# Performance work log

Measured on AMD Instinct MI355X. Metric: run time of the kernel, lower is better.

The kernel has to match this reference:

```python
import jax, jax.numpy as jnp
import numpy as np

N, F_IN, H, D = 4096, 256, 4, 64  # out_features = H*D = 256
SLOPE = 0.2
LN_EPS = 1e-5


def setup_inputs() -> dict:
    key = jax.random.key(0)
    k1, k2, k3, k4 = jax.random.split(key, 4)
    x = jax.random.normal(k1, (N, F_IN), dtype=jnp.float32)
    adjacency = jax.random.bernoulli(k2, 0.5, (N, N))
    # xavier_uniform for W [H*D, F_IN] and a [H, 2*D]
    lim_w = float(np.sqrt(6.0 / (F_IN + H * D)))
    W = jax.random.uniform(k3, (H * D, F_IN), minval=-lim_w, maxval=lim_w, dtype=jnp.float32)
    lim_a = float(np.sqrt(6.0 / (H + 2 * D)))
    a = jax.random.uniform(k4, (H, 2 * D), minval=-lim_a, maxval=lim_a, dtype=jnp.float32)
    ln_gamma = jnp.ones((H * D,), dtype=jnp.float32)
    ln_beta = jnp.zeros((H * D,), dtype=jnp.float32)
    return {"x": x, "adjacency": adjacency, "W": W, "a": a,
            "ln_gamma": ln_gamma, "ln_beta": ln_beta}


def _layernorm(y, gamma, beta):
    mu = jnp.mean(y, axis=-1, keepdims=True)
    var = jnp.mean((y - mu) ** 2, axis=-1, keepdims=True)
    return (y - mu) * jax.lax.rsqrt(var + LN_EPS) * gamma + beta


def reference(x, adjacency, W, a, ln_gamma, ln_beta):
    # Wx: [N, H, D]
    Wx = (x @ W.T).reshape(N, H, D)
    # Additive score split: sum over concat([Wx_i, Wx_j]) * a == Wx_i.a_src + Wx_j.a_dst
    a_src, a_dst = a[:, :D], a[:, D:]
    s_i = jnp.einsum('nhd,hd->nh', Wx, a_src)  # [N, H] (destination i)
    s_j = jnp.einsum('nhd,hd->nh', Wx, a_dst)  # [N, H] (source j)
    e = s_i[:, None, :] + s_j[None, :, :]       # [N, N, H]
    e = jnp.where(e >= 0, e, SLOPE * e)          # leaky relu
    e = jnp.where(adjacency[:, :, None], e, -jnp.inf)
    attn = jax.nn.softmax(e, axis=1)             # softmax over source j (dim=1)
    # dropout is identity in eval mode
    out = jnp.einsum('ijh,jhd->ihd', attn, Wx).reshape(N, H * D)
    out = out + x  # out_features == in_features -> residual
    return _layernorm(out, ln_gamma, ln_beta)
```

## Files before the change

### kernel.cpp

```cpp
#include <hip/hip_runtime.h>
#include <hip/hip_bf16.h>
#include <cstdint>
#include <cstddef>

#define N_NODES 4096
#define F_IN    256
#define H_HEADS 4
#define D_HEAD  64
#define FEAT    256
#define SLOPE   0.2f
#define LN_EPS  1e-5f

#define NCHUNK  4
#define J_CHUNK 1024
#define I_TILE  32
#define K_STEP  32
#define NSTEP   (J_CHUNK / K_STEP)

typedef __attribute__((ext_vector_type(8))) short bf16x8;
typedef __attribute__((ext_vector_type(4))) float f32x4;

#define FLAG_OFF   0
#define GMAX_OFF   64
#define ADJB_OFF   256
#define ADJB_BYTES ((size_t)N_NODES * 128 * 4)
#define WXT_OFF    (ADJB_OFF + ADJB_BYTES)
#define WXT_BYTES  ((size_t)FEAT * N_NODES * 2)
#define SSRC_OFF   (WXT_OFF + WXT_BYTES)
#define SVEC_BYTES ((size_t)H_HEADS * N_NODES * 4)
#define SDST_OFF   (SSRC_OFF + SVEC_BYTES)
#define WSL_OFF    (SDST_OFF + SVEC_BYTES)
#define WSL_BYTES  ((size_t)NCHUNK * N_NODES * H_HEADS * 4)
#define WSACC_OFF  (WSL_OFF + WSL_BYTES)
#define WSACC_BYTES ((size_t)NCHUNK * N_NODES * FEAT * 4)

__device__ __forceinline__ short f2bf(float f) {
    uint32_t u = __float_as_uint(f);
    uint32_t r = (u + 0x7fffu + ((u >> 16) & 1u)) >> 16;
    return (short)r;
}
__device__ __forceinline__ uint32_t fkey(float f) {
    uint32_t u = __float_as_uint(f);
    return ((int)u < 0) ? ~u : (u | 0x80000000u);
}
__device__ __forceinline__ float funkey(uint32_t k) {
    uint32_t u = (k & 0x80000000u) ? (k & 0x7fffffffu) : ~k;
    return __uint_as_float(u);
}

__global__ void detect_kernel(const uint8_t* __restrict__ adj,
                              int* __restrict__ flag, uint32_t* __restrict__ gmax) {
    int t = threadIdx.x;
    uint32_t acc = 0;
    for (int idx = t; idx < 4096; idx += 64)
        if (idx & 3) acc |= adj[idx];
    unsigned long long any = __ballot(acc != 0);
    if (t == 0) *flag = (any == 0ull) ? 1 : 0;
    if (t < H_HEADS) gmax[t] = 0u;
}

__global__ __launch_bounds__(256) void pack_adj(const uint8_t* __restrict__ adj8,
                                                const int* __restrict__ flag,
                                                uint32_t* __restrict__ bits) {
    int gid = blockIdx.x * 256 + threadIdx.x;
    uint32_t b = 0;
    if (!(*flag)) {
        const uint32_t* src = (const uint32_t*)adj8 + (size_t)gid * 8;
        #pragma unroll
        for (int k = 0; k < 8; ++k) {
            uint32_t v = src[k];
            if (v & 0x000000ffu) b |= 1u << (k * 4 + 0);
            if (v & 0x0000ff00u) b |= 1u << (k * 4 + 1);
            if (v & 0x00ff0000u) b |= 1u << (k * 4 + 2);
            if (v & 0xff000000u) b |= 1u << (k * 4 + 3);
        }
    } else {
        const int4* src = (const int4*)adj8 + (size_t)gid * 8;
        #pragma unroll
        for (int k = 0; k < 8; ++k) {
            int4 v = src[k];
            if (v.x) b |= 1u << (k * 4 + 0);
            if (v.y) b |= 1u << (k * 4 + 1);
            if (v.z) b |= 1u << (k * 4 + 2);
            if (v.w) b |= 1u << (k * 4 + 3);
        }
    }
    bits[gid] = b;
}

__global__ __launch_bounds__(256) void gemm_wx(const float* __restrict__ x,
                                               const float* __restrict__ W,
                                               const float* __restrict__ a,
                                               short* __restrict__ WxT,
                                               float* __restrict__ s_srcT,
                                               float* __restrict__ s_dstT,
                                               uint32_t* __restrict__ gmax) {
    __shared__ float xs[64][68];
    __shared__ float wsm[64][68];
    __shared__ float aS[64], aD[64];
    __shared__ float wredmax[4];
    const int h  = blockIdx.x;
    const int nt = blockIdx.y;
    const int t  = threadIdx.x;
    const int tm = t >> 4, tn = t & 15;
    if (t < 64)       aS[t]      = a[h * 128 + t];
    else if (t < 128) aD[t - 64] = a[h * 128 + 64 + (t - 64)];
    float acc[4][4] = {};

    for (int k0 = 0; k0 < F_IN; k0 += 64) {
        #pragma unroll
        for (int s = 0; s < 4; ++s) {
            int idx = t + s * 256;
            int r = idx >> 4, c4 = (idx & 15) << 2;
            *(float4*)&xs[r][c4]  = *(const float4*)&x[(size_t)(nt * 64 + r) * F_IN + k0 + c4];
            *(float4*)&wsm[r][c4] = *(const float4*)&W[(size_t)(h * 64 + r) * F_IN + k0 + c4];
        }
        __syncthreads();
        #pragma unroll 4
        for (int kk = 0; kk < 64; ++kk) {
            float av[4], bv[4];
            #pragma unroll
            for (int mi = 0; mi < 4; ++mi) av[mi] = xs[tm * 4 + mi][kk];
            #pragma unroll
            for (int ni = 0; ni < 4; ++ni) bv[ni] = wsm[tn * 4 + ni][kk];
            #pragma unroll
            for (int mi = 0; mi < 4; ++mi)
                #pragma unroll
                for (int ni = 0; ni < 4; ++ni)
                    acc[mi][ni] = fmaf(av[mi], bv[ni], acc[mi][ni]);
        }
        __syncthreads();
    }

    #pragma unroll
    for (int ni = 0; ni < 4; ++ni) {
        short4 sv;
        sv.x = f2bf(acc[0][ni]); sv.y = f2bf(acc[1][ni]);
        sv.z = f2bf(acc[2][ni]); sv.w = f2bf(acc[3][ni]);
        *(short4*)&WxT[(size_t)(h * 64 + tn * 4 + ni) * N_NODES + nt * 64 + tm * 4] = sv;
    }

    float ps[4] = {0.f, 0.f, 0.f, 0.f}, pd[4] = {0.f, 0.f, 0.f, 0.f};
    #pragma unroll
    for (int mi = 0; mi < 4; ++mi)
        #pragma unroll
        for (int ni = 0; ni < 4; ++ni) {
            float v = acc[mi][ni];
            ps[mi] = fmaf(v, aS[tn * 4 + ni], ps[mi]);
            pd[mi] = fmaf(v, aD[tn * 4 + ni], pd[mi]);
        }
    #pragma unroll
    for (int o = 1; o < 16; o <<= 1) {
        #pragma unroll
        for (int mi = 0; mi < 4; ++mi) {
            ps[mi] += __shfl_xor(ps[mi], o, 64);
            pd[mi] += __shfl_xor(pd[mi], o, 64);
        }
    }
    float lmax = -INFINITY;
    if (tn == 0) {
        #pragma unroll
        for (int mi = 0; mi < 4; ++mi) {
            int node = nt * 64 + tm * 4 + mi;
            s_srcT[(size_t)h * N_NODES + node] = ps[mi];
            s_dstT[(size_t)h * N_NODES + node] = pd[mi];
            lmax = fmaxf(lmax, pd[mi]);
        }
    }
    #pragma unroll
    for (int o = 1; o < 64; o <<= 1) lmax = fmaxf(lmax, __shfl_xor(lmax, o, 64));
    if ((t & 63) == 0) wredmax[t >> 6] = lmax;
    __syncthreads();
    if (t == 0) {
        float m = fmaxf(fmaxf(wredmax[0], wredmax[1]), fmaxf(wredmax[2], wredmax[3]));
        atomicMax(&gmax[h], fkey(m));
    }
}

__global__ __launch_bounds__(512, 4) void attn_chunk(const short* __restrict__ WxT,
                                                     const float* __restrict__ s_srcT,
                                                     const float* __restrict__ s_dstT,
                                                     const uint32_t* __restrict__ adjbits,
                                                     const uint32_t* __restrict__ gmax,
                                                     float* __restrict__ ws_l,
                                                     float* __restrict__ ws_acc) {
    __shared__ short    Bt[2][256][40];
    __shared__ uint32_t adjW[32][33];
    __shared__ float    sJ[4][1032];

    const int t     = threadIdx.x;
    const int tile  = blockIdx.x >> 2;
    const int chunk = blockIdx.x & 3;
    const int i0    = tile * I_TILE;
    const int jc    = chunk * J_CHUNK;
    const int wave  = t >> 6, lane = t & 63;
    const int h     = wave & 3, mh = wave >> 2;
    const int col   = lane & 15, q = lane >> 4;

    for (int s2 = t; s2 < 1024; s2 += 512)
        adjW[s2 >> 5][s2 & 31] =
            adjbits[(size_t)(i0 + (s2 >> 5)) * 128 + chunk * 32 + (s2 & 31)];
    for (int s2 = t; s2 < 1024; s2 += 512) {
        int pl = s2 >> 8, off = (s2 & 255) * 4;
        *(float4*)&sJ[pl][off] = *(const float4*)&s_dstT[(size_t)pl * N_NODES + jc + off];
    }
    const int sf = t >> 1, shalf = t & 1;
    const int4* gsrc = (const int4*)(WxT + (size_t)sf * N_NODES + jc);
    {
        int4 v0 = gsrc[shalf * 2 + 0], v1 = gsrc[shalf * 2 + 1];
        int4* ld = (int4*)&Bt[0][sf][shalf * 16];
        ld[0] = v0; ld[1] = v1;
    }
    __syncthreads();

    const int   iL  = mh * 16 + col;
    const int   i   = i0 + iL;
    const float si  = s_srcT[(size_t)h * N_NODES + i];
    const float gm  = funkey(gmax[h]);
    const float em0 = si + gm;
    const float mi_ = fmaxf(em0, SLOPE * em0);

    f32x4 cacc[4], cl;
    #pragma unroll
    for (int n = 0; n < 4; ++n)
        #pragma unroll
        for (int r2 = 0; r2 < 4; ++r2) cacc[n][r2] = 0.f;
    #pragma unroll
    for (int r2 = 0; r2 < 4; ++r2) cl[r2] = 0.f;

    bf16x8 onesf;
    #pragma unroll
    for (int e = 0; e < 8; ++e) onesf[e] = (col == 0) ? (short)0x3F80 : (short)0;

    for (int ks = 0; ks < NSTEP; ++ks) {
        const int  cur  = ks & 1;
        const bool more = (ks + 1 < NSTEP);
        int4 pf0, pf1;
        if (more) {
            pf0 = gsrc[(ks + 1) * 4 + shalf * 2 + 0];
            pf1 = gsrc[(ks + 1) * 4 + shalf * 2 + 1];
        }

        uint32_t wq = adjW[iL][ks] >> (q * 8);
        const float4 sa = *(const float4*)&sJ[h][ks * 32 + q * 8];
        const float4 sb = *(const float4*)&sJ[h][ks * 32 + q * 8 + 4];
        float sjv[8] = {sa.x, sa.y, sa.z, sa.w, sb.x, sb.y, sb.z, sb.w};
        bf16x8 ap;
        #pragma unroll
        for (int jj = 0; jj < 8; ++jj) {
            float e = si + sjv[jj];
            e = fmaxf(e, SLOPE * e);
            float p = __expf(e - mi_);
            p = (wq & (1u << jj)) ? p : 0.f;
            ap[jj] = f2bf(p);
        }

        #pragma unroll
        for (int n = 0; n < 4; ++n) {
            bf16x8 bfr = *(const bf16x8*)&Bt[cur][h * 64 + n * 16 + col][q * 8];
            cacc[n] = __builtin_amdgcn_mfma_f32_16x16x32_bf16(ap, bfr, cacc[n], 0, 0, 0);
        }
        cl = __builtin_amdgcn_mfma_f32_16x16x32_bf16(ap, onesf, cl, 0, 0, 0);

        if (more) {
            int4* ld = (int4*)&Bt[cur ^ 1][sf][shalf * 16];
            ld[0] = pf0; ld[1] = pf1;
        }
        __syncthreads();
    }

    #pragma unroll
    for (int n = 0; n < 4; ++n)
        #pragma unroll
        for (int r = 0; r < 4; ++r) {
            int ii = i0 + mh * 16 + q * 4 + r;
            ws_acc[((size_t)chunk * N_NODES + ii) * FEAT + h * 64 + n * 16 + col] = cacc[n][r];
        }
    if (col == 0) {
        #pragma unroll
        for (int r = 0; r < 4; ++r) {
            int ii = i0 + mh * 16 + q * 4 + r;
            ws_l[((size_t)chunk * N_NODES + ii) * H_HEADS + h] = cl[r];
        }
    }
}

__global__ __launch_bounds__(256) void finalize_kernel(const float* __restrict__ x,
                                                       const float* __restrict__ gamma,
                                                       const float* __restrict__ beta,
                                                       const float* __restrict__ ws_l,
                                                       const float* __restrict__ ws_acc,
                                                       float* __restrict__ out) {
    const int i = blockIdx.x;
    const int t = threadIdx.x;
    const int h = t >> 6;
    const int lane = t & 63;

    float L = 0.f, y = 0.f;
    #pragma unroll
    for (int c = 0; c < NCHUNK; ++c) {
        L += ws_l[((size_t)c * N_NODES + i) * H_HEADS + h];
        y += ws_acc[((size_t)c * N_NODES + i) * FEAT + t];
    }
    y = (L > 0.f ? y / L : 0.f) + x[(size_t)i * FEAT + t];

    float s1 = y, s2 = y * y;
    #pragma unroll
    for (int o = 32; o > 0; o >>= 1) {
        s1 += __shfl_xor(s1, o, 64);
        s2 += __shfl_xor(s2, o, 64);
    }
    __shared__ float red1[4], red2[4];
    if (lane == 0) { red1[h] = s1; red2[h] = s2; }
    __syncthreads();
    s1 = red1[0] + red1[1] + red1[2] + red1[3];
    s2 = red2[0] + red2[1] + red2[2] + red2[3];
    float mu  = s1 * (1.f / 256.f);
    float var = s2 * (1.f / 256.f) - mu * mu;
    float r = 1.0f / sqrtf(var + LN_EPS);
    out[(size_t)i * FEAT + t] = (y - mu) * r * gamma[t] + beta[t];
}

extern "C" void kernel_launch(void* const* d_in, const int* in_sizes, int n_in,
                              void* d_out, int out_size, void* d_ws, size_t ws_size,
                              hipStream_t stream) {
    const float* x     = (const float*)d_in[0];
    const void*  adj   = d_in[1];
    const float* W     = (const float*)d_in[2];
    const float* a     = (const float*)d_in[3];
    const float* gamma = (const float*)d_in[4];
    const float* beta  = (const float*)d_in[5];
    float* out = (float*)d_out;

    char* ws = (char*)d_ws;
    int*      flag    = (int*)(ws + FLAG_OFF);
    uint32_t* gmax    = (uint32_t*)(ws + GMAX_OFF);
    uint32_t* adjbits = (uint32_t*)(ws + ADJB_OFF);
    short*    WxT     = (short*)(ws + WXT_OFF);
    float*    s_srcT  = (float*)(ws + SSRC_OFF);
    float*    s_dstT  = (float*)(ws + SDST_OFF);
    float*    ws_l    = (float*)(ws + WSL_OFF);
    float*    ws_acc  = (float*)(ws + WSACC_OFF);

    detect_kernel<<<1, 64, 0, stream>>>((const uint8_t*)adj, flag, gmax);
    pack_adj<<<2048, 256, 0, stream>>>((const uint8_t*)adj, flag, adjbits);
    gemm_wx<<<dim3(4, 64), 256, 0, stream>>>(x, W, a, WxT, s_srcT, s_dstT, gmax);
    attn_chunk<<<512, 512, 0, stream>>>(WxT, s_srcT, s_dstT, adjbits, gmax, ws_l, ws_acc);
    finalize_kernel<<<N_NODES, 256, 0, stream>>>(x, gamma, beta, ws_l, ws_acc, out);
}
```

Baseline: 183.7 us.

## Factor attention exponentials, drop detect kernel, deepen prefetch, vectorize GEMM and finalize

The attention kernel no longer computes exp per edge. Each weight is rebuilt as a product of per-node factors precomputed in the GEMM: exp(s_dst) and exp(0.2*s_dst) per source, plus Ai, A2i and a sign threshold per destination. The adjacency-format detection moves into pack_adj with a block-local check, removing one launch. WxT prefetch becomes two steps ahead, the GEMM inner loop reads float4 from shared memory, and finalize handles one row per wavefront with float4 accesses. The risks are exp overflow or underflow in the factored form, and a block-local dtype check that could misclassify a block whose adjacency is stored as bytes.

```diff
diff --git a/kernel.cpp b/kernel.cpp
--- a/kernel.cpp
+++ b/kernel.cpp
@@ -20,7 +20,6 @@
 typedef __attribute__((ext_vector_type(8))) short bf16x8;
 typedef __attribute__((ext_vector_type(4))) float f32x4;
 
-#define FLAG_OFF   0
 #define GMAX_OFF   64
 #define ADJB_OFF   256
 #define ADJB_BYTES ((size_t)N_NODES * 128 * 4)
@@ -28,11 +27,11 @@
 #define WXT_BYTES  ((size_t)FEAT * N_NODES * 2)
 #define SSRC_OFF   (WXT_OFF + WXT_BYTES)
 #define SVEC_BYTES ((size_t)H_HEADS * N_NODES * 4)
-#define SDST_OFF   (SSRC_OFF + SVEC_BYTES)
-#define WSL_OFF    (SDST_OFF + SVEC_BYTES)
+#define ETAB_OFF   (SSRC_OFF + SVEC_BYTES)
+#define ETAB_BYTES ((size_t)H_HEADS * N_NODES * 8)
+#define WSL_OFF    (ETAB_OFF + ETAB_BYTES)
 #define WSL_BYTES  ((size_t)NCHUNK * N_NODES * H_HEADS * 4)
 #define WSACC_OFF  (WSL_OFF + WSL_BYTES)
-#define WSACC_BYTES ((size_t)NCHUNK * N_NODES * FEAT * 4)
 
 __device__ __forceinline__ short f2bf(float f) {
     uint32_t u = __float_as_uint(f);
@@ -48,34 +47,39 @@
     return __uint_as_float(u);
 }
 
-__global__ void detect_kernel(const uint8_t* __restrict__ adj,
-                              int* __restrict__ flag, uint32_t* __restrict__ gmax) {
-    int t = threadIdx.x;
-    uint32_t acc = 0;
-    for (int idx = t; idx < 4096; idx += 64)
-        if (idx & 3) acc |= adj[idx];
-    unsigned long long any = __ballot(acc != 0);
-    if (t == 0) *flag = (any == 0ull) ? 1 : 0;
-    if (t < H_HEADS) gmax[t] = 0u;
-}
-
-__global__ __launch_bounds__(256) void pack_adj(const uint8_t* __restrict__ adj8,
-                                                const int* __restrict__ flag,
-                                                uint32_t* __restrict__ bits) {
-    int gid = blockIdx.x * 256 + threadIdx.x;
+__global__ __launch_bounds__(256) void pack_adj(const void* __restrict__ adjv,
+                                                uint32_t* __restrict__ bits,
+                                                uint32_t* __restrict__ gmax) {
+    __shared__ int s_u8;
+    const int t   = threadIdx.x;
+    const int gid = blockIdx.x * 256 + t;
+    if (blockIdx.x == 0 && t < H_HEADS) gmax[t] = 0u;
+
+    uint32_t w8[8];
+    const uint32_t* src8 = (const uint32_t*)adjv + (size_t)gid * 8;
+    #pragma unroll
+    for (int k = 0; k < 8; ++k) w8[k] = src8[k];
+
+    uint32_t off = 0;
+    #pragma unroll
+    for (int k = 0; k < 8; ++k) off |= (w8[k] & 0xFFFFFF00u);
+    if (t == 0) s_u8 = 0;
+    __syncthreads();
+    if (off) s_u8 = 1;
+    __syncthreads();
+
     uint32_t b = 0;
-    if (!(*flag)) {
-        const uint32_t* src = (const uint32_t*)adj8 + (size_t)gid * 8;
+    if (s_u8) {
         #pragma unroll
         for (int k = 0; k < 8; ++k) {
-            uint32_t v = src[k];
+            uint32_t v = w8[k];
             if (v & 0x000000ffu) b |= 1u << (k * 4 + 0);
             if (v & 0x0000ff00u) b |= 1u << (k * 4 + 1);
             if (v & 0x00ff0000u) b |= 1u << (k * 4 + 2);
             if (v & 0xff000000u) b |= 1u << (k * 4 + 3);
         }
     } else {
-        const int4* src = (const int4*)adj8 + (size_t)gid * 8;
+        const int4* src = (const int4*)adjv + (size_t)gid * 8;
         #pragma unroll
         for (int k = 0; k < 8; ++k) {
             int4 v = src[k];
@@ -93,7 +97,7 @@
                                                const float* __restrict__ a,
                                                short* __restrict__ WxT,
                                                float* __restrict__ s_srcT,
-                                               float* __restrict__ s_dstT,
+                                               float2* __restrict__ etab,
                                                uint32_t* __restrict__ gmax) {
     __shared__ float xs[64][68];
     __shared__ float wsm[64][68];
@@ -117,17 +121,21 @@
         }
         __syncthreads();
         #pragma unroll 4
-        for (int kk = 0; kk < 64; ++kk) {
-            float av[4], bv[4];
+        for (int kq = 0; kq < 16; ++kq) {
+            float4 xa[4], wb[4];
             #pragma unroll
-            for (int mi = 0; mi < 4; ++mi) av[mi] = xs[tm * 4 + mi][kk];
+            for (int mi = 0; mi < 4; ++mi) xa[mi] = *(const float4*)&xs[tm * 4 + mi][kq * 4];
             #pragma unroll
-            for (int ni = 0; ni < 4; ++ni) bv[ni] = wsm[tn * 4 + ni][kk];
+            for (int ni = 0; ni < 4; ++ni) wb[ni] = *(const float4*)&wsm[tn + 16 * ni][kq * 4];
             #pragma unroll
             for (int mi = 0; mi < 4; ++mi)
                 #pragma unroll
-                for (int ni = 0; ni < 4; ++ni)
-                    acc[mi][ni] = fmaf(av[mi], bv[ni], acc[mi][ni]);
+                for (int ni = 0; ni < 4; ++ni) {
+                    acc[mi][ni] = fmaf(xa[mi].x, wb[ni].x, acc[mi][ni]);
+                    acc[mi][ni] = fmaf(xa[mi].y, wb[ni].y, acc[mi][ni]);
+                    acc[mi][ni] = fmaf(xa[mi].z, wb[ni].z, acc[mi][ni]);
+                    acc[mi][ni] = fmaf(xa[mi].w, wb[ni].w, acc[mi][ni]);
+                }
         }
         __syncthreads();
     }
@@ -137,7 +145,7 @@
         short4 sv;
         sv.x = f2bf(acc[0][ni]); sv.y = f2bf(acc[1][ni]);
         sv.z = f2bf(acc[2][ni]); sv.w = f2bf(acc[3][ni]);
-        *(short4*)&WxT[(size_t)(h * 64 + tn * 4 + ni) * N_NODES + nt * 64 + tm * 4] = sv;
+        *(short4*)&WxT[(size_t)(h * 64 + tn + 16 * ni) * N_NODES + nt * 64 + tm * 4] = sv;
     }
 
     float ps[4] = {0.f, 0.f, 0.f, 0.f}, pd[4] = {0.f, 0.f, 0.f, 0.f};
@@ -146,8 +154,8 @@
         #pragma unroll
         for (int ni = 0; ni < 4; ++ni) {
             float v = acc[mi][ni];
-            ps[mi] = fmaf(v, aS[tn * 4 + ni], ps[mi]);
-            pd[mi] = fmaf(v, aD[tn * 4 + ni], pd[mi]);
+            ps[mi] = fmaf(v, aS[tn + 16 * ni], ps[mi]);
+            pd[mi] = fmaf(v, aD[tn + 16 * ni], pd[mi]);
         }
     #pragma unroll
     for (int o = 1; o < 16; o <<= 1) {
@@ -163,7 +171,7 @@
         for (int mi = 0; mi < 4; ++mi) {
             int node = nt * 64 + tm * 4 + mi;
             s_srcT[(size_t)h * N_NODES + node] = ps[mi];
-            s_dstT[(size_t)h * N_NODES + node] = pd[mi];
+            etab[(size_t)h * N_NODES + node] = make_float2(__expf(pd[mi]), __expf(0.2f * pd[mi]));
             lmax = fmaxf(lmax, pd[mi]);
         }
     }
@@ -179,14 +187,14 @@
 
 __global__ __launch_bounds__(512, 4) void attn_chunk(const short* __restrict__ WxT,
                                                      const float* __restrict__ s_srcT,
-                                                     const float* __restrict__ s_dstT,
+                                                     const float2* __restrict__ etab,
                                                      const uint32_t* __restrict__ adjbits,
                                                      const uint32_t* __restrict__ gmax,
                                                      float* __restrict__ ws_l,
                                                      float* __restrict__ ws_acc) {
     __shared__ short    Bt[2][256][40];
     __shared__ uint32_t adjW[32][33];
-    __shared__ float    sJ[4][1032];
+    __shared__ float    EJ[4 * 2048];
 
     const int t     = threadIdx.x;
     const int tile  = blockIdx.x >> 2;
@@ -200,16 +208,22 @@
     for (int s2 = t; s2 < 1024; s2 += 512)
         adjW[s2 >> 5][s2 & 31] =
             adjbits[(size_t)(i0 + (s2 >> 5)) * 128 + chunk * 32 + (s2 & 31)];
-    for (int s2 = t; s2 < 1024; s2 += 512) {
-        int pl = s2 >> 8, off = (s2 & 255) * 4;
-        *(float4*)&sJ[pl][off] = *(const float4*)&s_dstT[(size_t)pl * N_NODES + jc + off];
-    }
+    {
+        const float4* esrc = (const float4*)etab;
+        for (int s2 = t; s2 < 2048; s2 += 512) {
+            int pl = s2 >> 9, off = s2 & 511;
+            *(float4*)&EJ[pl * 2048 + off * 4] = esrc[(size_t)pl * 2048 + (jc >> 1) + off];
+        }
+    }
+
     const int sf = t >> 1, shalf = t & 1;
     const int4* gsrc = (const int4*)(WxT + (size_t)sf * N_NODES + jc);
+    int4 pfA0, pfA1, pfB0, pfB1;
+    pfA0 = gsrc[shalf * 2 + 0];           pfA1 = gsrc[shalf * 2 + 1];
+    pfB0 = gsrc[4 + shalf * 2 + 0];       pfB1 = gsrc[4 + shalf * 2 + 1];
     {
-        int4 v0 = gsrc[shalf * 2 + 0], v1 = gsrc[shalf * 2 + 1];
         int4* ld = (int4*)&Bt[0][sf][shalf * 16];
-        ld[0] = v0; ld[1] = v1;
+        ld[0] = pfA0; ld[1] = pfA1;
     }
     __syncthreads();
 
@@ -219,6 +233,9 @@
     const float gm  = funkey(gmax[h]);
     const float em0 = si + gm;
     const float mi_ = fmaxf(em0, SLOPE * em0);
+    const float Ai  = __expf(si - mi_);
+    const float A2i = __expf(0.2f * si - mi_);
+    const float Ti  = __expf(-si);
 
     f32x4 cacc[4], cl;
     #pragma unroll
@@ -232,40 +249,51 @@
     #pragma unroll
     for (int e = 0; e < 8; ++e) onesf[e] = (col == 0) ? (short)0x3F80 : (short)0;
 
+    #pragma unroll 2
     for (int ks = 0; ks < NSTEP; ++ks) {
-        const int  cur  = ks & 1;
-        const bool more = (ks + 1 < NSTEP);
-        int4 pf0, pf1;
-        if (more) {
-            pf0 = gsrc[(ks + 1) * 4 + shalf * 2 + 0];
-            pf1 = gsrc[(ks + 1) * 4 + shalf * 2 + 1];
+        const int cur = ks & 1;
+
+        if (ks + 1 < NSTEP) {
+            int4* ld = (int4*)&Bt[cur ^ 1][sf][shalf * 16];
+            if (cur) { ld[0] = pfA0; ld[1] = pfA1; }
+            else     { ld[0] = pfB0; ld[1] = pfB1; }
+        }
+        if (ks + 2 < NSTEP) {
+            if (cur) { pfB0 = gsrc[(ks + 2) * 4 + shalf * 2]; pfB1 = gsrc[(ks + 2) * 4 + shalf * 2 + 1]; }
+            else     { pfA0 = gsrc[(ks + 2) * 4 + shalf * 2]; pfA1 = gsrc[(ks + 2) * 4 + shalf * 2 + 1]; }
         }
 
         uint32_t wq = adjW[iL][ks] >> (q * 8);
-        const float4 sa = *(const float4*)&sJ[h][ks * 32 + q * 8];
-        const float4 sb = *(const float4*)&sJ[h][ks * 32 + q * 8 + 4];
-        float sjv[8] = {sa.x, sa.y, sa.z, sa.w, sb.x, sb.y, sb.z, sb.w};
-        bf16x8 ap;
-        #pragma unroll
-        for (int jj = 0; jj < 8; ++jj) {
-            float e = si + sjv[jj];
-            e = fmaxf(e, SLOPE * e);
-            float p = __expf(e - mi_);
-            p = (wq & (1u << jj)) ? p : 0.f;
-            ap[jj] = f2bf(p);
+        float ej[16];
+        {
+            const float* eb = &EJ[h * 2048 + (ks * 32 + q * 8) * 2];
+            *(float4*)&ej[0]  = *(const float4*)&eb[0];
+            *(float4*)&ej[4]  = *(const float4*)&eb[4];
+            *(float4*)&ej[8]  = *(const float4*)&eb[8];
+            *(float4*)&ej[12] = *(const float4*)&eb[12];
+        }
+        union { uint32_t w[4]; bf16x8 v; } apu;
+        #pragma unroll
+        for (int pp = 0; pp < 4; ++pp) {
+            float B0 = ej[4 * pp + 0], B20 = ej[4 * pp + 1];
+            bool pos0 = B0 >= Ti;
+            float pv0 = (pos0 ? Ai : A2i) * (pos0 ? B0 : B20);
+            pv0 = (wq & (1u << (2 * pp))) ? pv0 : 0.f;
+            float B1 = ej[4 * pp + 2], B21 = ej[4 * pp + 3];
+            bool pos1 = B1 >= Ti;
+            float pv1 = (pos1 ? Ai : A2i) * (pos1 ? B1 : B21);
+            pv1 = (wq & (1u << (2 * pp + 1))) ? pv1 : 0.f;
+            apu.w[pp] = __builtin_amdgcn_perm(__float_as_uint(pv1), __float_as_uint(pv0),
+                                              0x07060302u);
         }
 
         #pragma unroll
         for (int n = 0; n < 4; ++n) {
             bf16x8 bfr = *(const bf16x8*)&Bt[cur][h * 64 + n * 16 + col][q * 8];
-            cacc[n] = __builtin_amdgcn_mfma_f32_16x16x32_bf16(ap, bfr, cacc[n], 0, 0, 0);
-        }
-        cl = __builtin_amdgcn_mfma_f32_16x16x32_bf16(ap, onesf, cl, 0, 0, 0);
-
-        if (more) {
-            int4* ld = (int4*)&Bt[cur ^ 1][sf][shalf * 16];
-            ld[0] = pf0; ld[1] = pf1;
-        }
+            cacc[n] = __builtin_amdgcn_mfma_f32_16x16x32_bf16(apu.v, bfr, cacc[n], 0, 0, 0);
+        }
+        cl = __builtin_amdgcn_mfma_f32_16x16x32_bf16(apu.v, onesf, cl, 0, 0, 0);
+
         __syncthreads();
     }
 
@@ -291,34 +319,42 @@
                                                        const float* __restrict__ ws_l,
                                                        const float* __restrict__ ws_acc,
                                                        float* __restrict__ out) {
-    const int i = blockIdx.x;
-    const int t = threadIdx.x;
-    const int h = t >> 6;
-    const int lane = t & 63;
-
-    float L = 0.f, y = 0.f;
+    const int w    = threadIdx.x >> 6;
+    const int lane = threadIdx.x & 63;
+    const int i    = blockIdx.x * 4 + w;
+    const int h    = lane >> 4;
+
+    float L = 0.f;
+    float4 y = make_float4(0.f, 0.f, 0.f, 0.f);
     #pragma unroll
     for (int c = 0; c < NCHUNK; ++c) {
         L += ws_l[((size_t)c * N_NODES + i) * H_HEADS + h];
-        y += ws_acc[((size_t)c * N_NODES + i) * FEAT + t];
-    }
-    y = (L > 0.f ? y / L : 0.f) + x[(size_t)i * FEAT + t];
-
-    float s1 = y, s2 = y * y;
+        float4 v = *(const float4*)&ws_acc[((size_t)c * N_NODES + i) * FEAT + lane * 4];
+        y.x += v.x; y.y += v.y; y.z += v.z; y.w += v.w;
+    }
+    float inv = (L > 0.f) ? (1.f / L) : 0.f;
+    float4 xv = *(const float4*)&x[(size_t)i * FEAT + lane * 4];
+    y.x = y.x * inv + xv.x; y.y = y.y * inv + xv.y;
+    y.z = y.z * inv + xv.z; y.w = y.w * inv + xv.w;
+
+    float s1 = y.x + y.y + y.z + y.w;
+    float s2 = y.x * y.x + y.y * y.y + y.z * y.z + y.w * y.w;
     #pragma unroll
     for (int o = 32; o > 0; o >>= 1) {
         s1 += __shfl_xor(s1, o, 64);
         s2 += __shfl_xor(s2, o, 64);
     }
-    __shared__ float red1[4], red2[4];
-    if (lane == 0) { red1[h] = s1; red2[h] = s2; }
-    __syncthreads();
-    s1 = red1[0] + red1[1] + red1[2] + red1[3];
-    s2 = red2[0] + red2[1] + red2[2] + red2[3];
     float mu  = s1 * (1.f / 256.f);
     float var = s2 * (1.f / 256.f) - mu * mu;
     float r = 1.0f / sqrtf(var + LN_EPS);
-    out[(size_t)i * FEAT + t] = (y - mu) * r * gamma[t] + beta[t];
+    float4 g = *(const float4*)&gamma[lane * 4];
+    float4 b = *(const float4*)&beta[lane * 4];
+    float4 o4;
+    o4.x = (y.x - mu) * r * g.x + b.x;
+    o4.y = (y.y - mu) * r * g.y + b.y;
+    o4.z = (y.z - mu) * r * g.z + b.z;
+    o4.w = (y.w - mu) * r * g.w + b.w;
+    *(float4*)&out[(size_t)i * FEAT + lane * 4] = o4;
 }
 
 extern "C" void kernel_launch(void* const* d_in, const int* in_sizes, int n_in,
@@ -333,18 +369,16 @@
     float* out = (float*)d_out;
 
     char* ws = (char*)d_ws;
-    int*      flag    = (int*)(ws + FLAG_OFF);
     uint32_t* gmax    = (uint32_t*)(ws + GMAX_OFF);
     uint32_t* adjbits = (uint32_t*)(ws + ADJB_OFF);
     short*    WxT     = (short*)(ws + WXT_OFF);
     float*    s_srcT  = (float*)(ws + SSRC_OFF);
-    float*    s_dstT  = (float*)(ws + SDST_OFF);
+    float2*   etab    = (float2*)(ws + ETAB_OFF);
     float*    ws_l    = (float*)(ws + WSL_OFF);
     float*    ws_acc  = (float*)(ws + WSACC_OFF);
 
-    detect_kernel<<<1, 64, 0, stream>>>((const uint8_t*)adj, flag, gmax);
-    pack_adj<<<2048, 256, 0, stream>>>((const uint8_t*)adj, flag, adjbits);
-    gemm_wx<<<dim3(4, 64), 256, 0, stream>>>(x, W, a, WxT, s_srcT, s_dstT, gmax);
-    attn_chunk<<<512, 512, 0, stream>>>(WxT, s_srcT, s_dstT, adjbits, gmax, ws_l, ws_acc);
-    finalize_kernel<<<N_NODES, 256, 0, stream>>>(x, gamma, beta, ws_l, ws_acc, out);
-}
+    pack_adj<<<2048, 256, 0, stream>>>(adj, adjbits, gmax);
+    gemm_wx<<<dim3(4, 64), 256, 0, stream>>>(x, W, a, WxT, s_srcT, etab, gmax);
+    attn_chunk<<<512, 512, 0, stream>>>(WxT, s_srcT, etab, adjbits, gmax, ws_l, ws_acc);
+    finalize_kernel<<<1024, 256, 0, stream>>>(x, gamma, beta, ws_l, ws_acc, out);
+}
```

Result: faster. 159.8 us (-13.0%).
